# Kernel tuning notes

Hardware: AMD Instinct MI355X
Metric: run time of the kernel (lower is better)

The kernel has to match this reference:

```python
import jax, jax.numpy as jnp
import numpy as np

MARGIN = 0.3
NEG_FILL = 1000000.0


def setup_inputs() -> dict:
    key = jax.random.key(0)
    k1, k2 = jax.random.split(key)
    features = jax.random.normal(k1, (8192, 128), dtype=jnp.float32)
    labels = jax.random.randint(k2, (8192,), 0, 512, dtype=jnp.int64)
    return {"features": features, "labels": labels}


def _triplet_loss(features, labels):
    N = features.shape[0]
    # pairwise euclidean distances via gram trick (matches torch.cdist p=2)
    sq = jnp.sum(features * features, axis=1)               # [N]
    d2 = sq[:, None] + sq[None, :] - 2.0 * (features @ features.T)
    d2 = jnp.maximum(d2, 0.0)
    # guard sqrt(0) on diagonal for clean gradients
    dist = jnp.where(d2 > 0.0, jnp.sqrt(jnp.where(d2 > 0.0, d2, 1.0)), 0.0)  # [N,N]

    same = labels[:, None] == labels[None, :]
    eye = jnp.eye(N, dtype=bool)
    is_pos = same & ~eye
    is_neg = ~same

    neg_inf = jnp.float32(-jnp.inf)
    pos_inf = jnp.float32(jnp.inf)
    has_pos = jnp.any(is_pos, axis=1)
    has_neg = jnp.any(is_neg, axis=1)
    # hardest positive: masked row max; empty -> 0.0
    dist_ap = jnp.max(jnp.where(is_pos, dist, neg_inf), axis=1)
    dist_ap = jnp.where(has_pos, dist_ap, 0.0)
    # hardest negative: masked row min; empty -> 1e6
    dist_an = jnp.min(jnp.where(is_neg, dist, pos_inf), axis=1)
    dist_an = jnp.where(has_neg, dist_an, NEG_FILL)

    # MarginRankingLoss with y=1: mean(max(0, margin - (dist_an - dist_ap)))
    return jnp.mean(jnp.maximum(0.0, MARGIN - (dist_an - dist_ap)))


def reference(features, labels):
    return _triplet_loss(features, labels)
```

## Files before the change

kernel.cpp:

```cpp
#include <hip/hip_runtime.h>
#include <hip/hip_bf16.h>
#include <math.h>

#define N 8192
#define D 128
#define MARGIN_V 0.3f
#define NEG_FILL 1000000.0f

typedef short bf16x8 __attribute__((ext_vector_type(8)));
typedef float f32x4  __attribute__((ext_vector_type(4)));


__global__ __launch_bounds__(256) void convert_kernel(const float* __restrict__ F,
                                                      unsigned short* __restrict__ Fb,
                                                      float* __restrict__ sq,
                                                      unsigned* __restrict__ ap,
                                                      unsigned* __restrict__ an) {
    __shared__ float red[16][17];
    const int g   = blockIdx.x;
    const int tid = threadIdx.x;
    const int q = tid >> 6, L = tid & 63;
    const int m = L & 15, j8 = (L >> 4) * 8;

    const float* src = F + (size_t)(16 * g + m) * D + 32 * q + j8;
    float4 v0 = *(const float4*)src;
    float4 v1 = *(const float4*)(src + 4);

    float s = v0.x * v0.x + v0.y * v0.y + v0.z * v0.z + v0.w * v0.w
            + v1.x * v1.x + v1.y * v1.y + v1.z * v1.z + v1.w * v1.w;

    union { bf16x8 v; __hip_bfloat162 h2[4]; } pk;
    pk.h2[0] = __float22bfloat162_rn({v0.x, v0.y});
    pk.h2[1] = __float22bfloat162_rn({v0.z, v0.w});
    pk.h2[2] = __float22bfloat162_rn({v1.x, v1.y});
    pk.h2[3] = __float22bfloat162_rn({v1.z, v1.w});
    *(bf16x8*)&Fb[(size_t)g * 2048 + tid * 8] = pk.v;

    red[m][q * 4 + (L >> 4)] = s;
    __syncthreads();
    if (tid < 16) {
        float t = 0.f;
        #pragma unroll
        for (int c = 0; c < 16; ++c) t += red[tid][c];
        sq[16 * g + tid] = t;
    }
    int gid = blockIdx.x * 256 + tid;
    if (gid < N) { ap[gid] = 0u; an[gid] = 0x7F800000u; }
}

__global__ __launch_bounds__(256, 2) void gemm_kernel(const unsigned short* __restrict__ Fb,
                                                      const float* __restrict__ sq,
                                                      const int* __restrict__ lab,
                                                      unsigned* __restrict__ ap,
                                                      unsigned* __restrict__ an) {
    const int tid  = threadIdx.x;
    const int wave = tid >> 6, lane = tid & 63;
    const int quad = lane >> 4, lr = lane & 15;
    const int S = blockIdx.x >> 4;
    const int C = blockIdx.x & 15;
    const int R0   = S * 256 + wave * 64;
    const int g0   = R0 >> 4;
    const int cg0  = C * 32;
    const int colb = C * 512;

    bf16x8 af[4][4];
    #pragma unroll
    for (int a = 0; a < 4; ++a)
        #pragma unroll
        for (int ks = 0; ks < 4; ++ks)
            af[a][ks] = *(const bf16x8*)&Fb[(((size_t)(g0 + a) * 4 + ks) * 64 + lane) * 8];

    f32x4 sqi4[4]; int4 labi4[4];
    #pragma unroll
    for (int a = 0; a < 4; ++a) {
        int base = R0 + a * 16 + quad * 4;
        sqi4[a]  = *(const f32x4*)&sq[base];
        labi4[a] = *(const int4*)&lab[base];
    }

    float rowP[4][4], rowN[4][4];
    #pragma unroll
    for (int a = 0; a < 4; ++a)
        #pragma unroll
        for (int r = 0; r < 4; ++r) { rowP[a][r] = -INFINITY; rowN[a][r] = INFINITY; }

#define LOADT(T, BF, SQJ, LABJ)                                                   \
    {                                                                             \
        _Pragma("unroll")                                                         \
        for (int b = 0; b < 2; ++b) {                                             \
            int gb = cg0 + 2 * (T) + b;                                           \
            _Pragma("unroll")                                                     \
            for (int ks = 0; ks < 4; ++ks)                                        \
                BF[b][ks] = *(const bf16x8*)&Fb[(((size_t)gb * 4 + ks) * 64 + lane) * 8]; \
            SQJ[b]  = sq[colb + (T) * 32 + b * 16 + lr];                          \
            LABJ[b] = lab[colb + (T) * 32 + b * 16 + lr];                         \
        }                                                                         \
    }

#define COMP(BF, SQJ, LABJ)                                                       \
    {                                                                             \
        f32x4 acc[4][2];                                                          \
        _Pragma("unroll")                                                         \
        for (int a = 0; a < 4; ++a)                                               \
            _Pragma("unroll")                                                     \
            for (int b = 0; b < 2; ++b) acc[a][b] = {0.f, 0.f, 0.f, 0.f};         \
        _Pragma("unroll")                                                         \
        for (int ks = 0; ks < 4; ++ks)                                            \
            _Pragma("unroll")                                                     \
            for (int a = 0; a < 4; ++a)                                           \
                _Pragma("unroll")                                                 \
                for (int b = 0; b < 2; ++b)                                       \
                    acc[a][b] = __builtin_amdgcn_mfma_f32_16x16x32_bf16(          \
                        af[a][ks], BF[b][ks], acc[a][b], 0, 0, 0);                \
        _Pragma("unroll")                                                         \
        for (int a = 0; a < 4; ++a)                                               \
            _Pragma("unroll")                                                     \
            for (int b = 0; b < 2; ++b)                                           \
                _Pragma("unroll")                                                 \
                for (int r = 0; r < 4; ++r) {                                     \
                    float u = fmaf(acc[a][b][r], -2.0f, SQJ[b]);                  \
                    bool same = (labi4[a][r] == LABJ[b]);                         \
                    rowP[a][r] = fmaxf(rowP[a][r], same ? u : -INFINITY);         \
                    rowN[a][r] = fminf(rowN[a][r], same ? INFINITY : u);          \
                }                                                                 \
    }

    bf16x8 b0[2][4], b1[2][4];
    float sq0[2], sq1[2];
    int   lb0[2], lb1[2];
    LOADT(0, b0, sq0, lb0);
    #pragma unroll 1
    for (int t = 0; t < 16; t += 2) {
        LOADT(t + 1, b1, sq1, lb1);
        COMP(b0, sq0, lb0);
        if (t + 2 < 16) LOADT(t + 2, b0, sq0, lb0);
        COMP(b1, sq1, lb1);
    }
#undef LOADT
#undef COMP

    #pragma unroll
    for (int a = 0; a < 4; ++a)
        #pragma unroll
        for (int r = 0; r < 4; ++r) {
            float p = rowP[a][r], n = rowN[a][r];
            #pragma unroll
            for (int off = 1; off < 16; off <<= 1) {
                p = fmaxf(p, __shfl_xor(p, off));
                n = fminf(n, __shfl_xor(n, off));
            }
            rowP[a][r] = p; rowN[a][r] = n;
        }
    if (lr == 0) {
        #pragma unroll
        for (int a = 0; a < 4; ++a)
            #pragma unroll
            for (int r = 0; r < 4; ++r) {
                int row = R0 + a * 16 + quad * 4 + r;
                float pd2 = fmaxf(sqi4[a][r] + rowP[a][r], 0.f);
                float nd2 = fmaxf(sqi4[a][r] + rowN[a][r], 0.f);
                atomicMax(&ap[row], __float_as_uint(pd2));
                atomicMin(&an[row], __float_as_uint(nd2));
            }
    }
}

__global__ __launch_bounds__(256) void loss_kernel(const float* __restrict__ ap,
                                                   const float* __restrict__ an,
                                                   float* __restrict__ out) {
    int tid = threadIdx.x;
    float sum = 0.f;
    #pragma unroll
    for (int k = 0; k < 8; ++k) {
        int i = k * 1024 + tid * 4;
        f32x4 a4 = *(const f32x4*)&ap[i];
        f32x4 n4 = *(const f32x4*)&an[i];
        #pragma unroll
        for (int c = 0; c < 4; ++c) {
            float apd = __builtin_amdgcn_sqrtf(a4[c]);
            float anv = n4[c];
            float and_ = (anv < INFINITY) ? __builtin_amdgcn_sqrtf(anv) : NEG_FILL;
            sum += fmaxf(0.f, MARGIN_V - (and_ - apd));
        }
    }
    #pragma unroll
    for (int off = 32; off >= 1; off >>= 1) sum += __shfl_xor(sum, off);
    __shared__ float s4[4];
    if ((tid & 63) == 0) s4[tid >> 6] = sum;
    __syncthreads();
    if (tid == 0) out[0] = (s4[0] + s4[1] + s4[2] + s4[3]) * (1.0f / (float)N);
}

extern "C" void kernel_launch(void* const* d_in, const int* in_sizes, int n_in,
                              void* d_out, int out_size, void* d_ws, size_t ws_size,
                              hipStream_t stream) {
    const float* F   = (const float*)d_in[0];
    const int*   lab = (const int*)d_in[1];

    unsigned short* Fb = (unsigned short*)d_ws;
    float*          sq = (float*)(Fb + (size_t)N * D);
    unsigned*       ap = (unsigned*)(sq + N);
    unsigned*       an = ap + N;

    convert_kernel<<<N / 16, 256, 0, stream>>>(F, Fb, sq, ap, an);
    gemm_kernel<<<512, 256, 0, stream>>>(Fb, sq, lab, ap, an);
    loss_kernel<<<1, 256, 0, stream>>>((const float*)ap, (const float*)an, (float*)d_out);
}
```

Before: 85.88 us.

## Halve per-wave row tile and double grid for higher occupancy

The distance GEMM kernel now gives each wave 32 rows instead of 64 and launches a 2D grid of 64x16 blocks, twice as many as before. Launch bounds are raised to 4 blocks per CU. The double-buffered B-tile pipeline is replaced by a single buffer whose next tile is prefetched after the MFMAs are issued, and the row squared norms are loaded only in the epilogue, all to cut register pressure. The aim is more resident waves to hide load latency, at the cost of fetching each column tile twice as often and having less MFMA work per load.

Measured after the change: 86.36 us. Within noise of the previous version (+0.6%).

```diff
diff --git a/kernel.cpp b/kernel.cpp
--- a/kernel.cpp
+++ b/kernel.cpp
@@ -48,7 +48,7 @@
     if (gid < N) { ap[gid] = 0u; an[gid] = 0x7F800000u; }
 }
 
-__global__ __launch_bounds__(256, 2) void gemm_kernel(const unsigned short* __restrict__ Fb,
+__global__ __launch_bounds__(256, 4) void gemm_kernel(const unsigned short* __restrict__ Fb,
                                                       const float* __restrict__ sq,
                                                       const int* __restrict__ lab,
                                                       unsigned* __restrict__ ap,
@@ -56,91 +56,88 @@
     const int tid  = threadIdx.x;
     const int wave = tid >> 6, lane = tid & 63;
     const int quad = lane >> 4, lr = lane & 15;
-    const int S = blockIdx.x >> 4;
-    const int C = blockIdx.x & 15;
-    const int R0   = S * 256 + wave * 64;
+    const int R0   = blockIdx.x * 128 + wave * 32;
     const int g0   = R0 >> 4;
-    const int cg0  = C * 32;
-    const int colb = C * 512;
-
-    bf16x8 af[4][4];
-    #pragma unroll
-    for (int a = 0; a < 4; ++a)
+    const int cg0  = blockIdx.y * 32;
+    const int colb = blockIdx.y * 512;
+
+    bf16x8 af[2][4];
+    #pragma unroll
+    for (int a = 0; a < 2; ++a)
         #pragma unroll
         for (int ks = 0; ks < 4; ++ks)
             af[a][ks] = *(const bf16x8*)&Fb[(((size_t)(g0 + a) * 4 + ks) * 64 + lane) * 8];
 
-    f32x4 sqi4[4]; int4 labi4[4];
-    #pragma unroll
-    for (int a = 0; a < 4; ++a) {
-        int base = R0 + a * 16 + quad * 4;
-        sqi4[a]  = *(const f32x4*)&sq[base];
-        labi4[a] = *(const int4*)&lab[base];
-    }
-
-    float rowP[4][4], rowN[4][4];
-    #pragma unroll
-    for (int a = 0; a < 4; ++a)
+    int4 labi4[2];
+    #pragma unroll
+    for (int a = 0; a < 2; ++a)
+        labi4[a] = *(const int4*)&lab[R0 + a * 16 + quad * 4];
+
+    float rowP[2][4], rowN[2][4];
+    #pragma unroll
+    for (int a = 0; a < 2; ++a)
         #pragma unroll
         for (int r = 0; r < 4; ++r) { rowP[a][r] = -INFINITY; rowN[a][r] = INFINITY; }
 
-#define LOADT(T, BF, SQJ, LABJ)                                                   \
-    {                                                                             \
-        _Pragma("unroll")                                                         \
-        for (int b = 0; b < 2; ++b) {                                             \
-            int gb = cg0 + 2 * (T) + b;                                           \
-            _Pragma("unroll")                                                     \
-            for (int ks = 0; ks < 4; ++ks)                                        \
-                BF[b][ks] = *(const bf16x8*)&Fb[(((size_t)gb * 4 + ks) * 64 + lane) * 8]; \
-            SQJ[b]  = sq[colb + (T) * 32 + b * 16 + lr];                          \
-            LABJ[b] = lab[colb + (T) * 32 + b * 16 + lr];                         \
-        }                                                                         \
-    }
-
-#define COMP(BF, SQJ, LABJ)                                                       \
-    {                                                                             \
-        f32x4 acc[4][2];                                                          \
-        _Pragma("unroll")                                                         \
-        for (int a = 0; a < 4; ++a)                                               \
-            _Pragma("unroll")                                                     \
-            for (int b = 0; b < 2; ++b) acc[a][b] = {0.f, 0.f, 0.f, 0.f};         \
-        _Pragma("unroll")                                                         \
-        for (int ks = 0; ks < 4; ++ks)                                            \
-            _Pragma("unroll")                                                     \
-            for (int a = 0; a < 4; ++a)                                           \
-                _Pragma("unroll")                                                 \
-                for (int b = 0; b < 2; ++b)                                       \
-                    acc[a][b] = __builtin_amdgcn_mfma_f32_16x16x32_bf16(          \
-                        af[a][ks], BF[b][ks], acc[a][b], 0, 0, 0);                \
-        _Pragma("unroll")                                                         \
-        for (int a = 0; a < 4; ++a)                                               \
-            _Pragma("unroll")                                                     \
-            for (int b = 0; b < 2; ++b)                                           \
-                _Pragma("unroll")                                                 \
-                for (int r = 0; r < 4; ++r) {                                     \
-                    float u = fmaf(acc[a][b][r], -2.0f, SQJ[b]);                  \
-                    bool same = (labi4[a][r] == LABJ[b]);                         \
-                    rowP[a][r] = fmaxf(rowP[a][r], same ? u : -INFINITY);         \
-                    rowN[a][r] = fminf(rowN[a][r], same ? INFINITY : u);          \
-                }                                                                 \
-    }
-
-    bf16x8 b0[2][4], b1[2][4];
-    float sq0[2], sq1[2];
-    int   lb0[2], lb1[2];
-    LOADT(0, b0, sq0, lb0);
+    bf16x8 bf[2][4];
+    float sqj[2], sqj_n[2];
+    int   labj[2], labj_n[2];
+
+    #pragma unroll
+    for (int b = 0; b < 2; ++b) {
+        int gb = cg0 + b;
+        #pragma unroll
+        for (int ks = 0; ks < 4; ++ks)
+            bf[b][ks] = *(const bf16x8*)&Fb[(((size_t)gb * 4 + ks) * 64 + lane) * 8];
+        sqj[b]  = sq[colb + b * 16 + lr];
+        labj[b] = lab[colb + b * 16 + lr];
+    }
+
     #pragma unroll 1
-    for (int t = 0; t < 16; t += 2) {
-        LOADT(t + 1, b1, sq1, lb1);
-        COMP(b0, sq0, lb0);
-        if (t + 2 < 16) LOADT(t + 2, b0, sq0, lb0);
-        COMP(b1, sq1, lb1);
-    }
-#undef LOADT
-#undef COMP
-
-    #pragma unroll
-    for (int a = 0; a < 4; ++a)
+    for (int t = 0; t < 16; ++t) {
+        f32x4 acc[2][2];
+        #pragma unroll
+        for (int a = 0; a < 2; ++a)
+            #pragma unroll
+            for (int b = 0; b < 2; ++b) acc[a][b] = {0.f, 0.f, 0.f, 0.f};
+        #pragma unroll
+        for (int ks = 0; ks < 4; ++ks)
+            #pragma unroll
+            for (int a = 0; a < 2; ++a)
+                #pragma unroll
+                for (int b = 0; b < 2; ++b)
+                    acc[a][b] = __builtin_amdgcn_mfma_f32_16x16x32_bf16(
+                        af[a][ks], bf[b][ks], acc[a][b], 0, 0, 0);
+
+        if (t < 15) {
+            #pragma unroll
+            for (int b = 0; b < 2; ++b) {
+                int gb = cg0 + 2 * (t + 1) + b;
+                #pragma unroll
+                for (int ks = 0; ks < 4; ++ks)
+                    bf[b][ks] = *(const bf16x8*)&Fb[(((size_t)gb * 4 + ks) * 64 + lane) * 8];
+                sqj_n[b]  = sq[colb + (t + 1) * 32 + b * 16 + lr];
+                labj_n[b] = lab[colb + (t + 1) * 32 + b * 16 + lr];
+            }
+        }
+
+        #pragma unroll
+        for (int a = 0; a < 2; ++a)
+            #pragma unroll
+            for (int b = 0; b < 2; ++b)
+                #pragma unroll
+                for (int r = 0; r < 4; ++r) {
+                    float u = fmaf(acc[a][b][r], -2.0f, sqj[b]);
+                    bool same = (labi4[a][r] == labj[b]);
+                    rowP[a][r] = fmaxf(rowP[a][r], same ? u : -INFINITY);
+                    rowN[a][r] = fminf(rowN[a][r], same ? INFINITY : u);
+                }
+        #pragma unroll
+        for (int b = 0; b < 2; ++b) { sqj[b] = sqj_n[b]; labj[b] = labj_n[b]; }
+    }
+
+    #pragma unroll
+    for (int a = 0; a < 2; ++a)
         #pragma unroll
         for (int r = 0; r < 4; ++r) {
             float p = rowP[a][r], n = rowN[a][r];
@@ -153,15 +150,17 @@
         }
     if (lr == 0) {
         #pragma unroll
-        for (int a = 0; a < 4; ++a)
+        for (int a = 0; a < 2; ++a) {
+            f32x4 sqi4 = *(const f32x4*)&sq[R0 + a * 16 + quad * 4];
             #pragma unroll
             for (int r = 0; r < 4; ++r) {
                 int row = R0 + a * 16 + quad * 4 + r;
-                float pd2 = fmaxf(sqi4[a][r] + rowP[a][r], 0.f);
-                float nd2 = fmaxf(sqi4[a][r] + rowN[a][r], 0.f);
+                float pd2 = fmaxf(sqi4[r] + rowP[a][r], 0.f);
+                float nd2 = fmaxf(sqi4[r] + rowN[a][r], 0.f);
                 atomicMax(&ap[row], __float_as_uint(pd2));
                 atomicMin(&an[row], __float_as_uint(nd2));
             }
+        }
     }
 }
 
@@ -203,6 +202,6 @@
     unsigned*       an = ap + N;
 
     convert_kernel<<<N / 16, 256, 0, stream>>>(F, Fb, sq, ap, an);
-    gemm_kernel<<<512, 256, 0, stream>>>(Fb, sq, lab, ap, an);
+    gemm_kernel<<<dim3(64, 16), 256, 0, stream>>>(Fb, sq, lab, ap, an);
     loss_kernel<<<1, 256, 0, stream>>>((const float*)ap, (const float*)an, (float*)d_out);
 }
```
